# Optimization experiments

Measured on AMD Instinct MI355X. Metric: run time of the kernel, lower is better.

## Reference

```python
import jax, jax.numpy as jnp
import numpy as np

HID = 128  # hidden_channel
C = 256    # feat_channel

def conv1x1(x, w, b):
    # x: [N, Cin, H, W], w: [Cout, Cin], b: [Cout]
    return jnp.einsum('nchw,oc->nohw', x, w) + b[None, :, None, None]

def maxpool2(x):
    N, Ch, H, W = x.shape
    return x.reshape(N, Ch, H // 2, 2, W // 2, 2).max(axis=(3, 5))

def setup_inputs() -> dict:
    key = jax.random.key(0)
    ks = jax.random.split(key, 6)
    rois = jax.random.normal(ks[0], (128, C, 14, 14), dtype=jnp.float32)
    feature = jax.random.normal(ks[1], (2, C, 64, 64), dtype=jnp.float32)
    s_in = 1.0 / np.sqrt(C)
    s_hid = 1.0 / np.sqrt(HID)
    wq = jax.random.uniform(ks[2], (HID, C), minval=-s_in, maxval=s_in, dtype=jnp.float32)
    wk = jax.random.uniform(ks[3], (HID, C), minval=-s_in, maxval=s_in, dtype=jnp.float32)
    wv = jax.random.uniform(ks[4], (HID, C), minval=-s_in, maxval=s_in, dtype=jnp.float32)
    wre = jax.random.uniform(ks[5], (C, HID), minval=-s_hid, maxval=s_hid, dtype=jnp.float32)
    return {
        'rois': rois, 'feature': feature,
        'wq': wq, 'bq': jnp.zeros((HID,), jnp.float32),
        'wk': wk, 'bk': jnp.zeros((HID,), jnp.float32),
        'wv': wv, 'bv': jnp.zeros((HID,), jnp.float32),
        'wre': wre, 'bre': jnp.zeros((C,), jnp.float32),
    }

def reference(rois, feature, wq, bq, wk, bk, wv, bv, wre, bre):
    BS_roinum, Cf, h, w = rois.shape
    BS = feature.shape[0]
    roinum = BS_roinum // BS
    _h, _w = h // 2, w // 2

    # Q at full resolution
    q = conv1x1(rois, wq, bq)                              # [BS*R, HID, h, w]
    q = q.transpose(0, 2, 3, 1).reshape(BS, roinum * h * w, HID)

    ds = maxpool2(rois)                                    # [BS*R, C, _h, _w]
    k = conv1x1(ds, wk, bk).transpose(0, 2, 3, 1).reshape(BS, roinum * _h * _w, HID)
    v = conv1x1(ds, wv, bv).transpose(0, 2, 3, 1).reshape(BS, roinum * _h * _w, HID)

    score = jnp.einsum('bqc,bkc->bqk', q, k)               # [BS, R*h*w, R*_h*_w]
    score = jax.nn.softmax(score, axis=-1)
    y = jnp.einsum('bqk,bkc->bqc', score, v)               # [BS, R*h*w, HID]

    y = y.reshape(BS * roinum, h, w, HID).transpose(0, 3, 1, 2)
    y = conv1x1(y, wre, bre)                               # [BS*R, C, h, w]
    return rois + y
```

## Files before the change

### kernel.cpp

```cpp
#include <hip/hip_runtime.h>
#include <math.h>

constexpr int CIN  = 256;
constexpr int HID  = 128;
constexpr int P    = 196;
constexpr int PP   = 49;
constexpr int NQ   = 12544;
constexpr int NKEY = 3136;

using f32x4 = __attribute__((ext_vector_type(4))) float;
using s16x8 = __attribute__((ext_vector_type(8))) short;
using s16x4 = __attribute__((ext_vector_type(4))) short;
using u32x2 = __attribute__((ext_vector_type(2))) unsigned int;

__device__ __forceinline__ unsigned short f2bf(float x) {
    unsigned int u = __float_as_uint(x);
    u += 0x7FFFu + ((u >> 16) & 1u);
    return (unsigned short)(u >> 16);
}
__device__ __forceinline__ float bf2f(unsigned short s) {
    return __uint_as_float(((unsigned int)s) << 16);
}

__global__ __launch_bounds__(256) void prep_kernel(
    const float* __restrict__ rois,
    const float* __restrict__ wq, const float* __restrict__ wk,
    const float* __restrict__ wv, const float* __restrict__ wre,
    unsigned short* __restrict__ xq, unsigned short* __restrict__ xkv,
    unsigned short* __restrict__ wqb, unsigned short* __restrict__ wkb,
    unsigned short* __restrict__ wvb, unsigned short* __restrict__ wreb)
{
    const int bx = blockIdx.x;
    const int t  = threadIdx.x;

    if (bx >= 512) {
        const int which = bx - 512;
        const float* src = (which == 0) ? wq : (which == 1) ? wk : (which == 2) ? wv : wre;
        unsigned short* dst = (which == 0) ? wqb : (which == 1) ? wkb
                             : (which == 2) ? wvb : wreb;
        #pragma unroll 4
        for (int i = 0; i < 32; ++i) {
            const int idx = i * 256 + t;
            const float4 v = ((const float4*)src)[idx];
            s16x4 o;
            o[0] = (short)f2bf(v.x); o[1] = (short)f2bf(v.y);
            o[2] = (short)f2bf(v.z); o[3] = (short)f2bf(v.w);
            *(s16x4*)(dst + idx * 4) = o;
        }
        return;
    }

    const int n = bx >> 2;
    const int g = bx & 3;
    const int b = n >> 6, r = n & 63;
    __shared__ float xT[196 * 68];

    const int c_loc = t >> 2;
    const int pq    = t & 3;

    const float4* row4 = (const float4*)(rois + ((size_t)n * CIN + g * 64 + c_loc) * P);
    #pragma unroll
    for (int j = 0; j < 13; ++j) {
        const int idx4 = pq + 4 * j;
        if (idx4 < 49) {
            const float4 v = row4[idx4];
            xT[(idx4 * 4 + 0) * 68 + c_loc] = v.x;
            xT[(idx4 * 4 + 1) * 68 + c_loc] = v.y;
            xT[(idx4 * 4 + 2) * 68 + c_loc] = v.z;
            xT[(idx4 * 4 + 3) * 68 + c_loc] = v.w;
        }
    }
    __syncthreads();

    #pragma unroll
    for (int i = 0; i < 7; ++i) {
        const int u = i * 256 + t;
        if (u < 1568) {
            const int px = u >> 3, ch8 = (u & 7) * 8;
            s16x8 o;
            #pragma unroll
            for (int e = 0; e < 8; ++e)
                o[e] = (short)f2bf(xT[px * 68 + ch8 + e]);
            *(s16x8*)(xq + ((size_t)b * NQ + r * P + px) * CIN + g * 64 + ch8) = o;
        }
    }
    #pragma unroll
    for (int i = 0; i < 2; ++i) {
        const int u = i * 256 + t;
        if (u < 392) {
            const int pp = u >> 3, ch8 = (u & 7) * 8;
            const int py = pp / 7, px_ = pp - py * 7;
            const int base00 = (py * 2) * 14 + px_ * 2;
            s16x8 o;
            #pragma unroll
            for (int e = 0; e < 8; ++e) {
                const int c = ch8 + e;
                const float m0 = fmaxf(xT[(base00)      * 68 + c], xT[(base00 + 1)  * 68 + c]);
                const float m1 = fmaxf(xT[(base00 + 14) * 68 + c], xT[(base00 + 15) * 68 + c]);
                o[e] = (short)f2bf(fmaxf(m0, m1));
            }
            *(s16x8*)(xkv + ((size_t)b * NKEY + r * PP + pp) * CIN + g * 64 + ch8) = o;
        }
    }
}

__global__ __launch_bounds__(256) void gemm_fused_kernel(
    const unsigned short* __restrict__ xq, const unsigned short* __restrict__ xkv,
    const unsigned short* __restrict__ wqb, const unsigned short* __restrict__ wkb,
    const unsigned short* __restrict__ wvb,
    const float* __restrict__ bq, const float* __restrict__ bk, const float* __restrict__ bv,
    unsigned short* __restrict__ q, unsigned short* __restrict__ kmat,
    unsigned short* __restrict__ vt_g)
{
    const int bx = blockIdx.x;
    const unsigned short* x; const unsigned short* w; const float* bias;
    int m_blk, mode;
    if (bx < 196)      { mode = 0; x = xq;  w = wqb; bias = bq; m_blk = bx; }
    else if (bx < 245) { mode = 1; x = xkv; w = wkb; bias = bk; m_blk = bx - 196; }
    else               { mode = 2; x = xkv; w = wvb; bias = bv; m_blk = bx - 245; }

    const int t = threadIdx.x;
    const int wid = t >> 6, lane = t & 63;
    const int quad = lane >> 4, c = lane & 15;
    const int m_base = m_blk * 128 + (wid & 1) * 64;
    const int n_base = (wid >> 1) * 64;

    f32x4 acc[4][4];
    #pragma unroll
    for (int i = 0; i < 4; ++i)
        #pragma unroll
        for (int j = 0; j < 4; ++j) acc[i][j] = (f32x4)(0.f);

    #pragma unroll
    for (int ks = 0; ks < 8; ++ks) {
        s16x8 af[4], bf[4];
        #pragma unroll
        for (int mt = 0; mt < 4; ++mt)
            af[mt] = *(const s16x8*)(x + (size_t)(m_base + mt * 16 + c) * CIN + ks * 32 + quad * 8);
        #pragma unroll
        for (int nt = 0; nt < 4; ++nt)
            bf[nt] = *(const s16x8*)(w + (size_t)(n_base + nt * 16 + c) * CIN + ks * 32 + quad * 8);
        #pragma unroll
        for (int mt = 0; mt < 4; ++mt)
            #pragma unroll
            for (int nt = 0; nt < 4; ++nt)
                acc[mt][nt] = __builtin_amdgcn_mfma_f32_16x16x32_bf16(af[mt], bf[nt], acc[mt][nt], 0, 0, 0);
    }

    if (mode <= 1) {
        unsigned short* out = (mode == 0) ? q : kmat;
        #pragma unroll
        for (int nt = 0; nt < 4; ++nt) {
            const float bv_ = bias[n_base + nt * 16 + c];
            #pragma unroll
            for (int mt = 0; mt < 4; ++mt)
                #pragma unroll
                for (int rr = 0; rr < 4; ++rr) {
                    const int m = m_base + mt * 16 + quad * 4 + rr;
                    out[(size_t)m * HID + n_base + nt * 16 + c] = f2bf(acc[mt][nt][rr] + bv_);
                }
        }
    } else {
        #pragma unroll
        for (int nt = 0; nt < 4; ++nt) {
            const int d = n_base + nt * 16 + c;
            const float bv_ = bias[d];
            #pragma unroll
            for (int mt = 0; mt < 4; ++mt)
                #pragma unroll
                for (int rr = 0; rr < 4; ++rr) {
                    const int key_g = m_base + mt * 16 + quad * 4 + rr;
                    const int bb = (key_g >= NKEY) ? 1 : 0;
                    const int kl = key_g - bb * NKEY;
                    vt_g[((size_t)bb * HID + d) * NKEY + kl] = f2bf(acc[mt][nt][rr] + bv_);
                }
        }
    }
}

__global__ __launch_bounds__(128, 2) void attn_kernel(
    const unsigned short* __restrict__ q, const unsigned short* __restrict__ kmat,
    const unsigned short* __restrict__ vt_g,
    unsigned short* __restrict__ opart, float* __restrict__ lpart)
{
    const int b    = blockIdx.y;
    const int s    = blockIdx.z;
    const int tid  = threadIdx.x;
    const int w    = tid >> 6;
    const int lane = tid & 63;
    const int quad = lane >> 4;
    const int c    = lane & 15;
    const int qb   = blockIdx.x * 128 + w * 64;

    __shared__ unsigned short Ps[2][64 * 72];

    const unsigned short* qg = q    + (size_t)b * NQ   * HID;
    const unsigned short* kg = kmat + (size_t)b * NKEY * HID;
    const unsigned short* vt = vt_g + (size_t)b * HID  * NKEY;

    s16x8 qf[4][4];
    #pragma unroll
    for (int nt = 0; nt < 4; ++nt)
        #pragma unroll
        for (int ks = 0; ks < 4; ++ks)
            qf[nt][ks] = *(const s16x8*)(qg + (size_t)(qb + nt * 16 + c) * HID + ks * 32 + quad * 8);

    f32x4 Ob[4][8];
    #pragma unroll
    for (int nt = 0; nt < 4; ++nt)
        #pragma unroll
        for (int nd = 0; nd < 8; ++nd) Ob[nt][nd] = (f32x4)(0.f);
    float l[4] = {0.f, 0.f, 0.f, 0.f};

    const int B6[6] = {0, 20, 40, 60, 79, 98};
    const int kt0 = B6[s], kt1 = B6[s + 1];

    for (int kt = kt0; kt < kt1; ++kt) {
        const int kb = kt * 32;

        f32x4 st[2][4];
        #pragma unroll
        for (int mt = 0; mt < 2; ++mt)
            #pragma unroll
            for (int nt = 0; nt < 4; ++nt) st[mt][nt] = (f32x4)(0.f);
        #pragma unroll
        for (int mt = 0; mt < 2; ++mt) {
            s16x8 kf[4];
            #pragma unroll
            for (int ks = 0; ks < 4; ++ks)
                kf[ks] = *(const s16x8*)(kg + (size_t)(kb + mt * 16 + c) * HID + ks * 32 + quad * 8);
            #pragma unroll
            for (int ks = 0; ks < 4; ++ks)
                #pragma unroll
                for (int nt = 0; nt < 4; ++nt)
                    st[mt][nt] = __builtin_amdgcn_mfma_f32_16x16x32_bf16(kf[ks], qf[nt][ks], st[mt][nt], 0, 0, 0);
        }

        #pragma unroll
        for (int mt = 0; mt < 2; ++mt) {
            #pragma unroll
            for (int nt = 0; nt < 4; ++nt) {
                const float e0 = __expf(st[mt][nt][0]);
                const float e1 = __expf(st[mt][nt][1]);
                const float e2 = __expf(st[mt][nt][2]);
                const float e3 = __expf(st[mt][nt][3]);
                l[nt] += (e0 + e1) + (e2 + e3);
                u32x2 pk;
                pk[0] = (unsigned int)f2bf(e0) | ((unsigned int)f2bf(e1) << 16);
                pk[1] = (unsigned int)f2bf(e2) | ((unsigned int)f2bf(e3) << 16);
                *(u32x2*)&Ps[w][(nt * 16 + c) * 72 + mt * 16 + quad * 4] = pk;
            }
        }

        s16x8 pf[4];
        #pragma unroll
        for (int nt = 0; nt < 4; ++nt)
            pf[nt] = *(const s16x8*)&Ps[w][(nt * 16 + c) * 72 + quad * 8];
        #pragma unroll
        for (int g2 = 0; g2 < 2; ++g2) {
            s16x8 vf[4];
            #pragma unroll
            for (int dd = 0; dd < 4; ++dd)
                vf[dd] = *(const s16x8*)(vt + (size_t)((g2 * 4 + dd) * 16 + c) * NKEY + kb + quad * 8);
            #pragma unroll
            for (int dd = 0; dd < 4; ++dd)
                #pragma unroll
                for (int nt = 0; nt < 4; ++nt)
                    Ob[nt][g2 * 4 + dd] = __builtin_amdgcn_mfma_f32_16x16x32_bf16(pf[nt], vf[dd], Ob[nt][g2 * 4 + dd], 0, 0, 0);
        }
    }

    unsigned short* Op = opart + (size_t)(s * 2 + b) * NQ * HID;
    #pragma unroll
    for (int nt = 0; nt < 4; ++nt) {
        #pragma unroll
        for (int nd = 0; nd < 8; ++nd) {
            #pragma unroll
            for (int rr = 0; rr < 4; ++rr) {
                const int qrow = qb + nt * 16 + quad * 4 + rr;
                Op[(size_t)qrow * HID + nd * 16 + c] = f2bf(Ob[nt][nd][rr]);
            }
        }
    }
    #pragma unroll
    for (int nt = 0; nt < 4; ++nt) {
        l[nt] += __shfl_xor(l[nt], 16, 64);
        l[nt] += __shfl_xor(l[nt], 32, 64);
    }
    if (quad == 0) {
        float* lp = lpart + (size_t)(s * 2 + b) * NQ;
        #pragma unroll
        for (int nt = 0; nt < 4; ++nt) lp[qb + nt * 16 + c] = l[nt];
    }
}

__global__ __launch_bounds__(256) void outproj_kernel(
    const float* __restrict__ rois,
    const unsigned short* __restrict__ opart, const float* __restrict__ lpart,
    const unsigned short* __restrict__ wreb, const float* __restrict__ bre,
    float* __restrict__ out)
{
    const int t = threadIdx.x;
    const int wid = t >> 6, lane = t & 63;
    const int quad = lane >> 4, c = lane & 15;
    const int m0 = blockIdx.x * 64;
    const int b  = (m0 >= NQ) ? 1 : 0;

    __shared__ unsigned short ys[64 * 136];

    {
        const int m_loc = t >> 2, kq = t & 3;
        const int q_local = (m0 + m_loc) - b * NQ;
        float lsum = 0.f;
        #pragma unroll
        for (int sl = 0; sl < 5; ++sl)
            lsum += lpart[(size_t)(sl * 2 + b) * NQ + q_local];
        const float invl = 1.0f / lsum;
        #pragma unroll
        for (int ch = 0; ch < 4; ++ch) {
            float a8[8] = {0, 0, 0, 0, 0, 0, 0, 0};
            #pragma unroll
            for (int sl = 0; sl < 5; ++sl) {
                const s16x8 v = *(const s16x8*)&opart[
                    ((size_t)(sl * 2 + b) * NQ + q_local) * HID + kq * 32 + ch * 8];
                #pragma unroll
                for (int e = 0; e < 8; ++e) a8[e] += bf2f((unsigned short)v[e]);
            }
            s16x8 o;
            #pragma unroll
            for (int e = 0; e < 8; ++e) o[e] = (short)f2bf(a8[e] * invl);
            *(s16x8*)&ys[m_loc * 136 + kq * 32 + ch * 8] = o;
        }
    }
    __syncthreads();

    const int o_base = wid * 64;
    s16x8 af[4][4];
    #pragma unroll
    for (int mt = 0; mt < 4; ++mt)
        #pragma unroll
        for (int ks = 0; ks < 4; ++ks)
            af[mt][ks] = *(const s16x8*)(wreb + (size_t)(o_base + mt * 16 + c) * HID + ks * 32 + quad * 8);

    f32x4 acc[4][4];
    #pragma unroll
    for (int i = 0; i < 4; ++i)
        #pragma unroll
        for (int j = 0; j < 4; ++j) acc[i][j] = (f32x4)(0.f);

    #pragma unroll
    for (int ks = 0; ks < 4; ++ks) {
        s16x8 bf[4];
        #pragma unroll
        for (int nt = 0; nt < 4; ++nt)
            bf[nt] = *(const s16x8*)&ys[(nt * 16 + c) * 136 + ks * 32 + quad * 8];
        #pragma unroll
        for (int mt = 0; mt < 4; ++mt)
            #pragma unroll
            for (int nt = 0; nt < 4; ++nt)
                acc[mt][nt] = __builtin_amdgcn_mfma_f32_16x16x32_bf16(af[mt][ks], bf[nt], acc[mt][nt], 0, 0, 0);
    }

    #pragma unroll
    for (int nt = 0; nt < 4; ++nt) {
        const int m_g = m0 + nt * 16 + c;
        const int mm  = m_g - b * NQ;
        const int r_roi = mm / 196;
        const int p     = mm - r_roi * 196;
        const int n_img = b * 64 + r_roi;
        const size_t base = ((size_t)n_img * CIN) * P + p;
        #pragma unroll
        for (int mt = 0; mt < 4; ++mt) {
            #pragma unroll
            for (int rr = 0; rr < 4; ++rr) {
                const int o = o_base + mt * 16 + quad * 4 + rr;
                out[base + (size_t)o * P] = rois[base + (size_t)o * P] + bre[o] + acc[mt][nt][rr];
            }
        }
    }
}

extern "C" void kernel_launch(void* const* d_in, const int* in_sizes, int n_in,
                              void* d_out, int out_size, void* d_ws, size_t ws_size,
                              hipStream_t stream)
{
    (void)in_sizes; (void)n_in; (void)out_size; (void)ws_size;
    const float* rois = (const float*)d_in[0];
    const float* wq  = (const float*)d_in[2];
    const float* bq  = (const float*)d_in[3];
    const float* wk  = (const float*)d_in[4];
    const float* bk  = (const float*)d_in[5];
    const float* wv  = (const float*)d_in[6];
    const float* bv  = (const float*)d_in[7];
    const float* wre = (const float*)d_in[8];
    const float* bre = (const float*)d_in[9];
    float* out = (float*)d_out;

    char* ws = (char*)d_ws;
    unsigned short* opart = (unsigned short*)(ws);
    unsigned short* xq    = (unsigned short*)(ws);
    unsigned short* xkv   = (unsigned short*)(ws + 12845056);
    unsigned short* wqb   = (unsigned short*)(ws + 16056320);
    unsigned short* wkb   = (unsigned short*)(ws + 16121856);
    unsigned short* wvb   = (unsigned short*)(ws + 16187392);
    unsigned short* q     = (unsigned short*)(ws + 32112640);
    unsigned short* kmat  = (unsigned short*)(ws + 38535168);
    unsigned short* vt_g  = (unsigned short*)(ws + 40140800);
    float*          lpart = (float*)         (ws + 41746432);
    unsigned short* wreb  = (unsigned short*)(ws + 42248192);

    prep_kernel<<<dim3(516), 256, 0, stream>>>(rois, wq, wk, wv, wre,
                                               xq, xkv, wqb, wkb, wvb, wreb);
    gemm_fused_kernel<<<dim3(294), 256, 0, stream>>>(xq, xkv, wqb, wkb, wvb,
                                                     bq, bk, bv, q, kmat, vt_g);
    attn_kernel<<<dim3(98, 2, 5), 128, 0, stream>>>(q, kmat, vt_g, opart, lpart);
    outproj_kernel<<<dim3(392), 256, 0, stream>>>(rois, opart, lpart, wreb, bre, out);
}
```

Baseline: 224.4 us.

## Stage K/V tiles in LDS with async double-buffered global_load_lds

The attention kernel now stages each 32-key K tile and V^T tile into swizzled, double-buffered LDS using direct global-to-LDS async loads, prefetching the next tile while computing the current one. Blocks grow to 4 waves (256 queries) sharing the staged tiles, and the key range is split 6 ways instead of 5. The workspace layout and the outproj reduction are adjusted to hold 6 partial outputs. This is meant to cut redundant global/L2 traffic for K and V across waves and to hide load latency, at the cost of more LDS and a barrier per tile.

Result: no change. 224.0 us (-0.2%).

```diff
diff --git a/kernel.cpp b/kernel.cpp
--- a/kernel.cpp
+++ b/kernel.cpp
@@ -7,11 +7,15 @@
 constexpr int PP   = 49;
 constexpr int NQ   = 12544;
 constexpr int NKEY = 3136;
+constexpr int NS   = 6;
 
 using f32x4 = __attribute__((ext_vector_type(4))) float;
 using s16x8 = __attribute__((ext_vector_type(8))) short;
 using s16x4 = __attribute__((ext_vector_type(4))) short;
 using u32x2 = __attribute__((ext_vector_type(2))) unsigned int;
+
+#define GLOBAL_AS(p) ((const void __attribute__((address_space(1)))*)(p))
+#define LDS_AS(p)    ((void __attribute__((address_space(3)))*)(p))
 
 __device__ __forceinline__ unsigned short f2bf(float x) {
     unsigned int u = __float_as_uint(x);
@@ -178,7 +182,7 @@
     }
 }
 
-__global__ __launch_bounds__(128, 2) void attn_kernel(
+__global__ __launch_bounds__(256, 2) void attn_kernel(
     const unsigned short* __restrict__ q, const unsigned short* __restrict__ kmat,
     const unsigned short* __restrict__ vt_g,
     unsigned short* __restrict__ opart, float* __restrict__ lpart)
@@ -190,14 +194,43 @@
     const int lane = tid & 63;
     const int quad = lane >> 4;
     const int c    = lane & 15;
-    const int qb   = blockIdx.x * 128 + w * 64;
-
-    __shared__ unsigned short Ps[2][64 * 72];
+    const int qb   = blockIdx.x * 256 + w * 64;
+
+    __shared__ unsigned short Kst[2][32 * 128];
+    __shared__ unsigned short Vst[2][128 * 32];
+    __shared__ unsigned short Ps[4][64 * 72];
 
     const unsigned short* qg = q    + (size_t)b * NQ   * HID;
     const unsigned short* kg = kmat + (size_t)b * NKEY * HID;
     const unsigned short* vt = vt_g + (size_t)b * HID  * NKEY;
 
+    int koff[2], voff[2];
+    #pragma unroll
+    for (int i = 0; i < 2; ++i) {
+        const int dstk = w * 2048 + (i * 64 + lane) * 16;
+        koff[i] = dstk ^ (((dstk >> 8) & 7) << 4);
+        const int chunk = i * 64 + lane;
+        const int d = w * 32 + (chunk >> 2), sl = chunk & 3;
+        voff[i] = d * (NKEY * 2) + ((sl ^ (d & 3)) * 16);
+    }
+    const char* kc = (const char*)kg;
+    const char* vc = (const char*)vt;
+
+    const int B7[7] = {0, 17, 34, 50, 66, 82, 98};
+    const int kt0 = B7[s], kt1 = B7[s + 1];
+
+    {
+        const char* ks_ = kc + (size_t)kt0 * 8192;
+        const char* vs_ = vc + (size_t)kt0 * 64;
+        #pragma unroll
+        for (int i = 0; i < 2; ++i) {
+            __builtin_amdgcn_global_load_lds(GLOBAL_AS(ks_ + koff[i]),
+                LDS_AS((char*)&Kst[0][0] + w * 2048 + i * 1024), 16, 0, 0);
+            __builtin_amdgcn_global_load_lds(GLOBAL_AS(vs_ + voff[i]),
+                LDS_AS((char*)&Vst[0][0] + w * 2048 + i * 1024), 16, 0, 0);
+        }
+    }
+
     s16x8 qf[4][4];
     #pragma unroll
     for (int nt = 0; nt < 4; ++nt)
@@ -212,11 +245,24 @@
         for (int nd = 0; nd < 8; ++nd) Ob[nt][nd] = (f32x4)(0.f);
     float l[4] = {0.f, 0.f, 0.f, 0.f};
 
-    const int B6[6] = {0, 20, 40, 60, 79, 98};
-    const int kt0 = B6[s], kt1 = B6[s + 1];
-
+    __syncthreads();
+
+    int buf = 0;
     for (int kt = kt0; kt < kt1; ++kt) {
-        const int kb = kt * 32;
+        if (kt + 1 < kt1) {
+            const char* ks_ = kc + (size_t)(kt + 1) * 8192;
+            const char* vs_ = vc + (size_t)(kt + 1) * 64;
+            #pragma unroll
+            for (int i = 0; i < 2; ++i) {
+                __builtin_amdgcn_global_load_lds(GLOBAL_AS(ks_ + koff[i]),
+                    LDS_AS((char*)&Kst[buf ^ 1][0] + w * 2048 + i * 1024), 16, 0, 0);
+                __builtin_amdgcn_global_load_lds(GLOBAL_AS(vs_ + voff[i]),
+                    LDS_AS((char*)&Vst[buf ^ 1][0] + w * 2048 + i * 1024), 16, 0, 0);
+            }
+        }
+
+        const char* Kb = (const char*)&Kst[buf][0];
+        const char* Vb = (const char*)&Vst[buf][0];
 
         f32x4 st[2][4];
         #pragma unroll
@@ -225,10 +271,11 @@
             for (int nt = 0; nt < 4; ++nt) st[mt][nt] = (f32x4)(0.f);
         #pragma unroll
         for (int mt = 0; mt < 2; ++mt) {
+            const int row = mt * 16 + c;
             s16x8 kf[4];
             #pragma unroll
             for (int ks = 0; ks < 4; ++ks)
-                kf[ks] = *(const s16x8*)(kg + (size_t)(kb + mt * 16 + c) * HID + ks * 32 + quad * 8);
+                kf[ks] = *(const s16x8*)(Kb + ((row * 256 + ks * 64 + quad * 16) ^ ((c & 7) << 4)));
             #pragma unroll
             for (int ks = 0; ks < 4; ++ks)
                 #pragma unroll
@@ -260,14 +307,19 @@
         for (int g2 = 0; g2 < 2; ++g2) {
             s16x8 vf[4];
             #pragma unroll
-            for (int dd = 0; dd < 4; ++dd)
-                vf[dd] = *(const s16x8*)(vt + (size_t)((g2 * 4 + dd) * 16 + c) * NKEY + kb + quad * 8);
+            for (int dd = 0; dd < 4; ++dd) {
+                const int d = (g2 * 4 + dd) * 16 + c;
+                vf[dd] = *(const s16x8*)(Vb + (d * 64 + ((quad ^ (d & 3)) * 16)));
+            }
             #pragma unroll
             for (int dd = 0; dd < 4; ++dd)
                 #pragma unroll
                 for (int nt = 0; nt < 4; ++nt)
                     Ob[nt][g2 * 4 + dd] = __builtin_amdgcn_mfma_f32_16x16x32_bf16(pf[nt], vf[dd], Ob[nt][g2 * 4 + dd], 0, 0, 0);
         }
+
+        if (kt + 1 < kt1) __syncthreads();
+        buf ^= 1;
     }
 
     unsigned short* Op = opart + (size_t)(s * 2 + b) * NQ * HID;
@@ -313,14 +365,14 @@
         const int q_local = (m0 + m_loc) - b * NQ;
         float lsum = 0.f;
         #pragma unroll
-        for (int sl = 0; sl < 5; ++sl)
+        for (int sl = 0; sl < NS; ++sl)
             lsum += lpart[(size_t)(sl * 2 + b) * NQ + q_local];
         const float invl = 1.0f / lsum;
         #pragma unroll
         for (int ch = 0; ch < 4; ++ch) {
             float a8[8] = {0, 0, 0, 0, 0, 0, 0, 0};
             #pragma unroll
-            for (int sl = 0; sl < 5; ++sl) {
+            for (int sl = 0; sl < NS; ++sl) {
                 const s16x8 v = *(const s16x8*)&opart[
                     ((size_t)(sl * 2 + b) * NQ + q_local) * HID + kq * 32 + ch * 8];
                 #pragma unroll
@@ -403,16 +455,16 @@
     unsigned short* wqb   = (unsigned short*)(ws + 16056320);
     unsigned short* wkb   = (unsigned short*)(ws + 16121856);
     unsigned short* wvb   = (unsigned short*)(ws + 16187392);
-    unsigned short* q     = (unsigned short*)(ws + 32112640);
-    unsigned short* kmat  = (unsigned short*)(ws + 38535168);
-    unsigned short* vt_g  = (unsigned short*)(ws + 40140800);
-    float*          lpart = (float*)         (ws + 41746432);
-    unsigned short* wreb  = (unsigned short*)(ws + 42248192);
+    unsigned short* q     = (unsigned short*)(ws + 38535168);
+    unsigned short* kmat  = (unsigned short*)(ws + 44957696);
+    unsigned short* vt_g  = (unsigned short*)(ws + 46563328);
+    float*          lpart = (float*)         (ws + 48168960);
+    unsigned short* wreb  = (unsigned short*)(ws + 48771072);
 
     prep_kernel<<<dim3(516), 256, 0, stream>>>(rois, wq, wk, wv, wre,
                                                xq, xkv, wqb, wkb, wvb, wreb);
     gemm_fused_kernel<<<dim3(294), 256, 0, stream>>>(xq, xkv, wqb, wkb, wvb,
                                                      bq, bk, bv, q, kmat, vt_g);
-    attn_kernel<<<dim3(98, 2, 5), 128, 0, stream>>>(q, kmat, vt_g, opart, lpart);
+    attn_kernel<<<dim3(49, 2, NS), 256, 0, stream>>>(q, kmat, vt_g, opart, lpart);
     outproj_kernel<<<dim3(392), 256, 0, stream>>>(rois, opart, lpart, wreb, bre, out);
 }
```
